# Kernel optimization log

Hardware: AMD Instinct MI355X
Metric: run time of the kernel (lower is better)

## Reference

```python
import jax, jax.numpy as jnp
import numpy as np

B, T, U, V = 8, 128, 64, 512
BLANK = 0
NEG_INF = -1e30  # finite 'log zero' to keep gradients NaN-free


def setup_inputs() -> dict:
    key = jax.random.key(0)
    k1, k2, k3, k4, k5 = jax.random.split(key, 5)
    emissions = jax.random.normal(k1, (B, T, V), dtype=jnp.float32)
    predictions = jax.random.normal(k2, (B, U, V), dtype=jnp.float32)
    labels = jax.random.randint(k3, (B, U - 1), 1, V, dtype=jnp.int32)
    # max(input_lengths) must equal T; max(label_lengths) must equal U-1
    input_lengths = jax.random.randint(k4, (B,), T // 2, T + 1, dtype=jnp.int32).at[0].set(T)
    label_lengths = jax.random.randint(k5, (B,), (U - 1) // 2, U, dtype=jnp.int32).at[0].set(U - 1)
    return {
        "emissions": emissions,
        "predictions": predictions,
        "labels": labels,
        "input_lengths": input_lengths,
        "label_lengths": label_lengths,
    }


def _rnnt_costs(emissions, predictions, labels, input_lengths, label_lengths, blank=BLANK):
    b, t_len, v = emissions.shape
    u_len = predictions.shape[1]
    # joint lattice log-probs: log_softmax over vocab of additive joint
    log_probs = jax.nn.log_softmax(
        emissions[:, :, None, :] + predictions[:, None, :, :], axis=-1
    )  # (B, T, U, V)
    blank_lp = log_probs[..., blank]  # (B, T, U)
    lbl = jnp.broadcast_to(labels[:, None, :, None], (b, t_len, u_len - 1, 1))
    label_lp = jnp.take_along_axis(log_probs[:, :, : u_len - 1, :], lbl, axis=3)[..., 0]  # (B,T,U-1)

    def step(a_top, xs):
        # a_top[b,u] = alpha[t-1,u] + blank_lp[t-1,u]  (entry-from-above scores)
        blank_t, label_t = xs  # (B,U), (B,U-1)
        # c[u] = sum_{k<u} label_lp[t,k]  -> alpha[t,u] = c[u] + LSE_{u'<=u}(a_top[u'] - c[u'])
        c = jnp.concatenate(
            [jnp.zeros((b, 1), a_top.dtype), jnp.cumsum(label_t, axis=1)], axis=1
        )  # (B, U)
        alpha_t = c + jax.lax.cumlogsumexp(a_top - c, axis=1)
        a_next = alpha_t + blank_t  # alpha[t,u] + blank_lp[t,u]
        return a_next, a_next

    a0 = jnp.full((b, u_len), NEG_INF, dtype=emissions.dtype).at[:, 0].set(0.0)
    xs = (jnp.moveaxis(blank_lp, 1, 0), jnp.moveaxis(label_lp, 1, 0))
    _, scores = jax.lax.scan(step, a0, xs)  # (T, B, U): alpha[t,u]+blank_lp[t,u]
    scores = jnp.moveaxis(scores, 1, 0)  # (B, T, U)
    bidx = jnp.arange(b)
    # cost_b = -(alpha[T_b-1, U_b] + blank_lp[T_b-1, U_b])
    costs = -scores[bidx, input_lengths - 1, label_lengths]
    return costs


def reference(emissions, predictions, labels, input_lengths, label_lengths):
    return _rnnt_costs(emissions, predictions, labels, input_lengths, label_lengths)
```

## Files before the change

### kernel.cpp

```cpp
#include <hip/hip_runtime.h>

#define B 8
#define T 128
#define U 64
#define V 512
#define ROWS (T + 2)
#define PADK 520
#define LN2 0.6931471805599453f

typedef __attribute__((ext_vector_type(8))) short bf8v;
typedef __attribute__((ext_vector_type(4))) float f4v;

template<int CTRL, int ROWM>
__device__ __forceinline__ float dpp_movf(float x, int old_bits) {
    int r = __builtin_amdgcn_update_dpp(old_bits, __builtin_bit_cast(int, x),
                                        CTRL, ROWM, 0xF, false);
    return __builtin_bit_cast(float, r);
}
__device__ __forceinline__ float wave_max63(float x) {
    const int NI = (int)0xff800000u;
    x = fmaxf(x, dpp_movf<0x111, 0xF>(x, NI));
    x = fmaxf(x, dpp_movf<0x112, 0xF>(x, NI));
    x = fmaxf(x, dpp_movf<0x114, 0xF>(x, NI));
    x = fmaxf(x, dpp_movf<0x118, 0xF>(x, NI));
    x = fmaxf(x, dpp_movf<0x142, 0xA>(x, NI));
    x = fmaxf(x, dpp_movf<0x143, 0xC>(x, NI));
    return x;
}
__device__ __forceinline__ float rdlane(float x, int lane) {
    return __builtin_bit_cast(float,
        __builtin_amdgcn_readlane(__builtin_bit_cast(int, x), lane));
}
__device__ __forceinline__ float dpp_shr1(float x) {
    int r = __builtin_amdgcn_update_dpp(0, __builtin_bit_cast(int, x),
                                        0x138, 0xF, 0xF, false);
    return __builtin_bit_cast(float, r);
}

__device__ __forceinline__ short f2bf(float x) {
    unsigned b = __builtin_bit_cast(unsigned, x);
    unsigned r = (b + 0x7FFFu + ((b >> 16) & 1u)) >> 16;
    return (short)r;
}
__device__ __forceinline__ float bf2f(short h) {
    return __builtin_bit_cast(float, ((unsigned)(unsigned short)h) << 16);
}

__global__ __launch_bounds__(256) void fused_kernel(
    const float* __restrict__ em, const float* __restrict__ pr,
    const int* __restrict__ labels,
    const int* __restrict__ in_len, const int* __restrict__ lab_len,
    float* __restrict__ out)
{
    __shared__ __align__(16) char smemRaw[2 * 64 * PADK * 2];
    __shared__ float Pp0s[U], Ppls[U], Ee0s[T];
    __shared__ int   lbls[U];

    short*  Ph = (short*)smemRaw;
    short*  Pl = Ph + 64 * PADK;
    float2* QI = (float2*)smemRaw;

    const int b    = blockIdx.x;
    const int tid  = threadIdx.x;
    const int lane = tid & 63;
    const int w    = tid >> 6;

    if (tid < T)     Ee0s[tid] = __expf(em[((size_t)b * T + tid) * V]);
    if (tid < U)     Pp0s[tid] = __expf(pr[((size_t)b * U + tid) * V]);
    if (tid < U - 1) {
        const int lb = labels[b * (U - 1) + tid];
        lbls[tid] = lb;
        Ppls[tid] = __expf(pr[((size_t)b * U + tid) * V + lb]);
    }

    for (int idx = tid; idx < 64 * 64; idx += 256) {
        const int u = idx >> 6, c = idx & 63;
        const float* prow = pr + ((size_t)b * U + u) * V + c * 8;
        const float4 f0 = ((const float4*)prow)[0];
        const float4 f1 = ((const float4*)prow)[1];
        const float e[8] = {f0.x, f0.y, f0.z, f0.w, f1.x, f1.y, f1.z, f1.w};
        bf8v hi, lo;
        #pragma unroll
        for (int j = 0; j < 8; ++j) {
            const float x = __expf(e[j]);
            const short h = f2bf(x);
            hi[j] = h;
            lo[j] = f2bf(x - bf2f(h));
        }
        ((bf8v*)Ph)[u * (PADK / 8) + c] = hi;
        ((bf8v*)Pl)[u * (PADK / 8) + c] = lo;
    }
    __syncthreads();

    f4v acc[2][4];
    #pragma unroll
    for (int i = 0; i < 2; ++i)
        #pragma unroll
        for (int n = 0; n < 4; ++n) acc[i][n] = (f4v){0.f, 0.f, 0.f, 0.f};

    const int arow = lane & 15;
    const int kb   = (lane >> 4) * 8;

    #pragma unroll
    for (int mtl = 0; mtl < 2; ++mtl) {
        const int t = (w * 2 + mtl) * 16 + arow;
        const float* erow = em + ((size_t)b * T + t) * V;
        #pragma unroll 2
        for (int ks = 0; ks < 16; ++ks) {
            const int k0 = ks * 32 + kb;
            const float4 f0 = ((const float4*)(erow + k0))[0];
            const float4 f1 = ((const float4*)(erow + k0))[1];
            const float e[8] = {f0.x, f0.y, f0.z, f0.w, f1.x, f1.y, f1.z, f1.w};
            bf8v ah, al;
            #pragma unroll
            for (int j = 0; j < 8; ++j) {
                const float x = __expf(e[j]);
                const short h = f2bf(x);
                ah[j] = h;
                al[j] = f2bf(x - bf2f(h));
            }
            #pragma unroll
            for (int nt = 0; nt < 4; ++nt) {
                const int bu = nt * 16 + arow;
                const bf8v bh = ((const bf8v*)Ph)[bu * (PADK / 8) + k0 / 8];
                const bf8v bl = ((const bf8v*)Pl)[bu * (PADK / 8) + k0 / 8];
                acc[mtl][nt] = __builtin_amdgcn_mfma_f32_16x16x32_bf16(ah, bh, acc[mtl][nt], 0, 0, 0);
                acc[mtl][nt] = __builtin_amdgcn_mfma_f32_16x16x32_bf16(ah, bl, acc[mtl][nt], 0, 0, 0);
                acc[mtl][nt] = __builtin_amdgcn_mfma_f32_16x16x32_bf16(al, bh, acc[mtl][nt], 0, 0, 0);
            }
        }
    }
    __syncthreads();

    for (int i = tid; i < ROWS * U; i += 256) QI[i] = make_float2(0.f, 0.f);
    __syncthreads();

    const int ccol  = lane & 15;
    const int crow0 = (lane >> 4) * 4;
    #pragma unroll
    for (int mtl = 0; mtl < 2; ++mtl) {
        #pragma unroll
        for (int nt = 0; nt < 4; ++nt) {
            const int u = nt * 16 + ccol;
            #pragma unroll
            for (int r = 0; r < 4; ++r) {
                const int t = (w * 2 + mtl) * 16 + crow0 + r;
                const float inv = 1.0f / acc[mtl][nt][r];
                QI[(t + 1) * U + u].x = Ee0s[t] * Pp0s[u] * inv;
                if (u < U - 1) {
                    const float eel = __expf(em[((size_t)b * T + t) * V + lbls[u]]);
                    QI[t * U + (u + 1)].y = eel * Ppls[u] * inv;
                }
            }
        }
    }
    __syncthreads();
    if (tid >= 64) return;

    const int u  = tid;
    const int Tb = in_len[b];
    const int Ub = lab_len[b];
    const int dmax = (Tb - 1) + Ub;

    auto qidx = [&](int d) {
        int r = d - u;
        r = min(max(r, 0), T + 1);
        return r * U + u;
    };

    float A = (u == 0) ? 1.0f : 0.0f;
    int   off = 0;
    float aCap = 1.0f;
    int   offCap = 0;
    float sPend = 1.0f;
    int   ePend = 0;

    float2 c8[8], n8[8];
    #pragma unroll
    for (int j = 0; j < 8; ++j) c8[j] = QI[qidx(1 + j)];

    for (int d0 = 1; d0 <= 185; d0 += 8) {
        #pragma unroll
        for (int j = 0; j < 8; ++j) {
            n8[j] = QI[qidx(d0 + 8 + j)];
            A = fmaf(A, c8[j].x, dpp_shr1(A) * c8[j].y);
            if ((j & 3) == 3) {
                A *= sPend;
                off += ePend;
                const float mx = rdlane(wave_max63(A), 63);
                int e = ((__builtin_bit_cast(int, mx) >> 23) & 255) - 127;
                e = max(e, -96);
                sPend = __builtin_bit_cast(float, (157 - e) << 23);
                ePend = e - 30;
            }
            const bool cap = (d0 + j == dmax);
            aCap   = cap ? A   : aCap;
            offCap = cap ? off : offCap;
        }
        #pragma unroll
        for (int j = 0; j < 8; ++j) c8[j] = n8[j];
    }

    if (u == Ub) {
        const float bprob = QI[Tb * U + u].x;
        out[b] = -(__log2f(aCap) + (float)offCap + __log2f(bprob)) * LN2;
    }
}

extern "C" void kernel_launch(void* const* d_in, const int* in_sizes, int n_in,
                              void* d_out, int out_size, void* d_ws, size_t ws_size,
                              hipStream_t stream) {
    const float* em      = (const float*)d_in[0];
    const float* pr      = (const float*)d_in[1];
    const int*   labels  = (const int*)d_in[2];
    const int*   in_len  = (const int*)d_in[3];
    const int*   lab_len = (const int*)d_in[4];
    float* out = (float*)d_out;

    fused_kernel<<<B, 256, 0, stream>>>(em, pr, labels, in_len, lab_len, out);
}
```

Baseline: 33.86 us.

## Raise block to 1024 threads and split MFMA tiles across 16 waves

Raises the block from 4 waves to 16 waves. Each wave now computes one 16-row M tile over two N tiles instead of two M tiles over four N tiles, so the normalizer GEMM and the Q-table build are spread across four times as many waves within each batch's single block. The goal is more latency hiding and less serial work per wave in the pre-recurrence phase, given only 8 blocks exist. In exchange, each emission row's exp/bf16-split conversion is now done by two waves instead of one, and the 1024-thread launch bound limits registers per thread.

```diff
diff --git a/kernel.cpp b/kernel.cpp
--- a/kernel.cpp
+++ b/kernel.cpp
@@ -46,7 +46,7 @@
     return __builtin_bit_cast(float, ((unsigned)(unsigned short)h) << 16);
 }
 
-__global__ __launch_bounds__(256) void fused_kernel(
+__global__ __launch_bounds__(1024) void fused_kernel(
     const float* __restrict__ em, const float* __restrict__ pr,
     const int* __restrict__ labels,
     const int* __restrict__ in_len, const int* __restrict__ lab_len,
@@ -73,7 +73,7 @@
         Ppls[tid] = __expf(pr[((size_t)b * U + tid) * V + lb]);
     }
 
-    for (int idx = tid; idx < 64 * 64; idx += 256) {
+    for (int idx = tid; idx < 64 * 64; idx += 1024) {
         const int u = idx >> 6, c = idx & 63;
         const float* prow = pr + ((size_t)b * U + u) * V + c * 8;
         const float4 f0 = ((const float4*)prow)[0];
@@ -92,18 +92,17 @@
     }
     __syncthreads();
 
-    f4v acc[2][4];
-    #pragma unroll
-    for (int i = 0; i < 2; ++i)
-        #pragma unroll
-        for (int n = 0; n < 4; ++n) acc[i][n] = (f4v){0.f, 0.f, 0.f, 0.f};
+    f4v acc[2];
+    acc[0] = (f4v){0.f, 0.f, 0.f, 0.f};
+    acc[1] = (f4v){0.f, 0.f, 0.f, 0.f};
 
     const int arow = lane & 15;
     const int kb   = (lane >> 4) * 8;
-
-    #pragma unroll
-    for (int mtl = 0; mtl < 2; ++mtl) {
-        const int t = (w * 2 + mtl) * 16 + arow;
+    const int mt   = w >> 1;
+    const int nb   = (w & 1) * 2;
+
+    {
+        const int t = mt * 16 + arow;
         const float* erow = em + ((size_t)b * T + t) * V;
         #pragma unroll 2
         for (int ks = 0; ks < 16; ++ks) {
@@ -120,37 +119,34 @@
                 al[j] = f2bf(x - bf2f(h));
             }
             #pragma unroll
-            for (int nt = 0; nt < 4; ++nt) {
-                const int bu = nt * 16 + arow;
+            for (int j = 0; j < 2; ++j) {
+                const int bu = (nb + j) * 16 + arow;
                 const bf8v bh = ((const bf8v*)Ph)[bu * (PADK / 8) + k0 / 8];
                 const bf8v bl = ((const bf8v*)Pl)[bu * (PADK / 8) + k0 / 8];
-                acc[mtl][nt] = __builtin_amdgcn_mfma_f32_16x16x32_bf16(ah, bh, acc[mtl][nt], 0, 0, 0);
-                acc[mtl][nt] = __builtin_amdgcn_mfma_f32_16x16x32_bf16(ah, bl, acc[mtl][nt], 0, 0, 0);
-                acc[mtl][nt] = __builtin_amdgcn_mfma_f32_16x16x32_bf16(al, bh, acc[mtl][nt], 0, 0, 0);
-            }
-        }
-    }
-    __syncthreads();
-
-    for (int i = tid; i < ROWS * U; i += 256) QI[i] = make_float2(0.f, 0.f);
+                acc[j] = __builtin_amdgcn_mfma_f32_16x16x32_bf16(ah, bh, acc[j], 0, 0, 0);
+                acc[j] = __builtin_amdgcn_mfma_f32_16x16x32_bf16(ah, bl, acc[j], 0, 0, 0);
+                acc[j] = __builtin_amdgcn_mfma_f32_16x16x32_bf16(al, bh, acc[j], 0, 0, 0);
+            }
+        }
+    }
+    __syncthreads();
+
+    for (int i = tid; i < ROWS * U; i += 1024) QI[i] = make_float2(0.f, 0.f);
     __syncthreads();
 
     const int ccol  = lane & 15;
     const int crow0 = (lane >> 4) * 4;
     #pragma unroll
-    for (int mtl = 0; mtl < 2; ++mtl) {
-        #pragma unroll
-        for (int nt = 0; nt < 4; ++nt) {
-            const int u = nt * 16 + ccol;
-            #pragma unroll
-            for (int r = 0; r < 4; ++r) {
-                const int t = (w * 2 + mtl) * 16 + crow0 + r;
-                const float inv = 1.0f / acc[mtl][nt][r];
-                QI[(t + 1) * U + u].x = Ee0s[t] * Pp0s[u] * inv;
-                if (u < U - 1) {
-                    const float eel = __expf(em[((size_t)b * T + t) * V + lbls[u]]);
-                    QI[t * U + (u + 1)].y = eel * Ppls[u] * inv;
-                }
+    for (int j = 0; j < 2; ++j) {
+        const int u = (nb + j) * 16 + ccol;
+        #pragma unroll
+        for (int r = 0; r < 4; ++r) {
+            const int t = mt * 16 + crow0 + r;
+            const float inv = 1.0f / acc[j][r];
+            QI[(t + 1) * U + u].x = Ee0s[t] * Pp0s[u] * inv;
+            if (u < U - 1) {
+                const float eel = __expf(em[((size_t)b * T + t) * V + lbls[u]]);
+                QI[t * U + (u + 1)].y = eel * Ppls[u] * inv;
             }
         }
     }
@@ -217,5 +213,5 @@
     const int*   lab_len = (const int*)d_in[4];
     float* out = (float*)d_out;
 
-    fused_kernel<<<B, 256, 0, stream>>>(em, pr, labels, in_len, lab_len, out);
-}
+    fused_kernel<<<B, 1024, 0, stream>>>(em, pr, labels, in_len, lab_len, out);
+}
```

Result: no change. 34.35 us (+1.4%).
